# Performance work log

Measured on AMD Instinct MI355X. Metric: run time of the kernel, lower is better.

The kernel has to match this reference:

```python
import jax, jax.numpy as jnp
import numpy as np

N_NODES = 50000
N_EDGES = 800000
D = 128            # input_dim == output_dim (no zero-padding branch in GatedGraphConv)
N_ETYPES = 4
N_STEPS = 8
B = 50
MAX_NODES = 1400
HID = 256


def setup_inputs() -> dict:
    key = jax.random.key(0)
    ks = jax.random.split(key, 10)
    # ragged graph sizes: alternating 600 / 1400 nodes, sums exactly to N_NODES
    counts = np.tile(np.array([600, 1400], dtype=np.int32), B // 2)
    s_d = 1.0 / np.sqrt(D)
    s_h = 1.0 / np.sqrt(HID)
    return {
        "node_features": jax.random.normal(ks[0], (N_NODES, D), jnp.float32),
        "edge_src": jax.random.randint(ks[1], (N_EDGES,), 0, N_NODES, dtype=jnp.int32),
        "edge_dst": jax.random.randint(ks[2], (N_EDGES,), 0, N_NODES, dtype=jnp.int32),
        "edge_types": jax.random.randint(ks[3], (N_EDGES,), 0, N_ETYPES, dtype=jnp.int32),
        "node_counts": jnp.asarray(counts),
        # per-edge-type message linears (DGL: one nn.Linear(out,out) per etype)
        "W_msg": jax.random.normal(ks[4], (N_ETYPES, D, D), jnp.float32) * s_d,
        "b_msg": jnp.zeros((N_ETYPES, D), jnp.float32),
        # GRUCell params (torch gate order: r, z, n)
        "W_ih": jax.random.normal(ks[5], (3 * D, D), jnp.float32) * s_d,
        "W_hh": jax.random.normal(ks[6], (3 * D, D), jnp.float32) * s_d,
        "b_ih": jnp.zeros((3 * D,), jnp.float32),
        "b_hh": jnp.zeros((3 * D,), jnp.float32),
        # classifier: Linear(D,256) + ReLU + Linear(256,1) + sigmoid (dropout = identity at eval)
        "W1": jax.random.normal(ks[7], (D, HID), jnp.float32) * s_d,
        "b1": jnp.zeros((HID,), jnp.float32),
        "W2": jax.random.normal(ks[8], (HID, 1), jnp.float32) * s_h,
        "b2": jnp.zeros((1,), jnp.float32),
    }


def _forward(node_features, edge_src, edge_dst, edge_types, node_counts,
             W_msg, b_msg, W_ih, W_hh, b_ih, b_hh, W1, b1, W2, b2):
    h = node_features
    for _ in range(N_STEPS):
        h_src = h[edge_src]                                   # [E, D] gather
        m = jnp.zeros_like(h_src)
        for t in range(N_ETYPES):                             # small fixed loop over edge types
            m = m + jnp.where((edge_types == t)[:, None],
                              h_src @ W_msg[t] + b_msg[t], 0.0)
        a = jax.ops.segment_sum(m, edge_dst, num_segments=N_NODES)  # [N, D] scatter-sum
        # GRUCell update
        gi = a @ W_ih.T + b_ih
        gh = h @ W_hh.T + b_hh
        i_r, i_z, i_n = jnp.split(gi, 3, axis=-1)
        h_r, h_z, h_n = jnp.split(gh, 3, axis=-1)
        r = jax.nn.sigmoid(i_r + h_r)
        z = jax.nn.sigmoid(i_z + h_z)
        n = jnp.tanh(i_n + r * h_n)
        h = (1.0 - z) * n + z * h
    # de-batchify to padded [B, MAX_NODES, D] + masked mean pool
    offsets = jnp.concatenate([jnp.zeros((1,), node_counts.dtype),
                               jnp.cumsum(node_counts)[:-1]])
    idx = offsets[:, None] + jnp.arange(MAX_NODES, dtype=node_counts.dtype)
    mask = jnp.arange(MAX_NODES)[None, :] < node_counts[:, None]
    g = h[jnp.clip(idx, 0, N_NODES - 1)] * mask[..., None]    # [B, MAX_NODES, D]
    pooled = g.sum(axis=1) / node_counts[:, None].astype(h.dtype)
    x = jax.nn.relu(pooled @ W1 + b1)
    return jax.nn.sigmoid(x @ W2 + b2)                        # [B, 1]


def reference(node_features, edge_src, edge_dst, edge_types, node_counts,
              W_msg, b_msg, W_ih, W_hh, b_ih, b_hh, W1, b1, W2, b2):
    return _forward(node_features, edge_src, edge_dst, edge_types, node_counts,
                    W_msg, b_msg, W_ih, W_hh, b_ih, b_hh, W1, b1, W2, b2)
```

## Files before the change

kernel.cpp:

```cpp
#include <hip/hip_runtime.h>
#include <hip/hip_bf16.h>

#define N_NODES 50000
#define N_EDGES 800000
#define D 128
#define N_ETYPES 4
#define N_STEPS 8
#define B_GRAPHS 50
#define HID 256
#define POOL_SPLIT 16
#define N4 (N_NODES * N_ETYPES)
#define SCAN_B4 ((N4 + 255) / 256)

typedef __attribute__((ext_vector_type(8))) short short8;
typedef __attribute__((ext_vector_type(4))) float f32x4;
typedef __attribute__((ext_vector_type(4))) unsigned uint4v;
typedef __attribute__((ext_vector_type(4))) int int4v;

static __device__ __forceinline__ unsigned short f2bf(float f) {
    union { float f; unsigned u; } v; v.f = f;
    unsigned r = v.u + 0x7FFF + ((v.u >> 16) & 1);
    return (unsigned short)(r >> 16);
}
static __device__ __forceinline__ unsigned pk2(float a, float b) {
    return (unsigned)f2bf(a) | ((unsigned)f2bf(b) << 16);
}
static __device__ __forceinline__ float bf2f_u(unsigned s) {
    union { unsigned u; float f; } v; v.u = s << 16;
    return v.f;
}
static __device__ __forceinline__ float bflo(unsigned x) {
    union { unsigned u; float f; } v; v.u = x << 16;
    return v.f;
}
static __device__ __forceinline__ float bfhi(unsigned x) {
    union { unsigned u; float f; } v; v.u = x & 0xFFFF0000u;
    return v.f;
}
static __device__ __forceinline__ float fsigmoid(float x) {
    return 1.f / (1.f + __expf(-x));
}
static __device__ __forceinline__ float ftanh(float x) {
    return 2.f / (1.f + __expf(-2.f * x)) - 1.f;
}

__global__ void k_init_h(const float* __restrict__ nf, unsigned short* __restrict__ hbf) {
    int i = blockIdx.x * blockDim.x + threadIdx.x;
    if (i < N_NODES * D) hbf[i] = f2bf(nf[i]);
}

__global__ void k_hist(const int* __restrict__ dst, const int* __restrict__ et,
                       int* __restrict__ deg4) {
    int e = blockIdx.x * blockDim.x + threadIdx.x;
    if (e < N_EDGES) atomicAdd(&deg4[dst[e] * 4 + et[e]], 1);
}

__global__ __launch_bounds__(256) void k_scan1(const int* __restrict__ deg4,
                                               int* __restrict__ bsum) {
    __shared__ int tmp[256];
    int t = threadIdx.x;
    int i = blockIdx.x * 256 + t;
    tmp[t] = (i < N4) ? deg4[i] : 0;
    __syncthreads();
    for (int s = 128; s > 0; s >>= 1) {
        if (t < s) tmp[t] += tmp[t + s];
        __syncthreads();
    }
    if (t == 0) bsum[blockIdx.x] = tmp[0];
}

__global__ __launch_bounds__(1024) void k_scan2(const int* __restrict__ bsum,
                                                int* __restrict__ bpfx,
                                                int* __restrict__ rowptr4) {
    __shared__ int part[1024];
    int t = threadIdx.x;
    int v = (t < SCAN_B4) ? bsum[t] : 0;
    part[t] = v;
    __syncthreads();
    for (int off = 1; off < 1024; off <<= 1) {
        int u = (t >= off) ? part[t - off] : 0;
        __syncthreads();
        part[t] += u;
        __syncthreads();
    }
    if (t < SCAN_B4) bpfx[t] = part[t] - v;
    if (t == SCAN_B4 - 1) rowptr4[N4] = part[t];
}

__global__ __launch_bounds__(256) void k_scan3(const int* __restrict__ deg4,
                                               const int* __restrict__ bpfx,
                                               int* __restrict__ rowptr4,
                                               int* __restrict__ cursor4) {
    __shared__ int part[256];
    int t = threadIdx.x;
    int i = blockIdx.x * 256 + t;
    int v = (i < N4) ? deg4[i] : 0;
    part[t] = v;
    __syncthreads();
    for (int off = 1; off < 256; off <<= 1) {
        int u = (t >= off) ? part[t - off] : 0;
        __syncthreads();
        part[t] += u;
        __syncthreads();
    }
    if (i < N4) {
        int rp = bpfx[blockIdx.x] + part[t] - v;
        rowptr4[i] = rp;
        cursor4[i] = rp;
    }
}

__global__ void k_fill(const int* __restrict__ src, const int* __restrict__ dst,
                       const int* __restrict__ et, int* __restrict__ cursor4,
                       int* __restrict__ epack) {
    int e = blockIdx.x * blockDim.x + threadIdx.x;
    if (e < N_EDGES) {
        int slot = atomicAdd(&cursor4[dst[e] * 4 + et[e]], 1);
        epack[slot] = src[e] << 8;
    }
}

__global__ void k_pack(const float* __restrict__ Wmsg, const float* __restrict__ Wih,
                       const float* __restrict__ Whh, unsigned short* __restrict__ Pmsg,
                       unsigned short* __restrict__ Pih, unsigned short* __restrict__ Phh) {
    int bt = blockIdx.x;
    int l = threadIdx.x;
    if (bt < 128) {
        int nt = bt >> 4, kc = bt & 15;
        int n = nt * 16 + (l & 15);
        unsigned short* out = Pmsg + (((size_t)bt * 64 + l) * 8);
#pragma unroll
        for (int i = 0; i < 8; ++i) {
            int k = kc * 32 + ((l >> 4) << 3) + i;
            out[i] = f2bf(Wmsg[(size_t)(k >> 7) * (D * D) + (k & 127) * D + n]);
        }
        return;
    }
    const float* src;
    unsigned short* dstp;
    int id;
    if (bt < 224) { id = bt - 128; src = Wih; dstp = Pih; }
    else          { id = bt - 224; src = Whh; dstp = Phh; }
    int nt = id >> 2, c = id & 3;
    int n = nt * 16 + (l & 15);
    unsigned short* out = dstp + (((size_t)(nt * 4 + c) * 64 + l) * 8);
#pragma unroll
    for (int i = 0; i < 8; ++i) {
        int k = c * 32 + ((l >> 4) << 3) + i;
        out[i] = f2bf(src[n * D + k]);
    }
}

__global__ void k_pack_bias(const float* __restrict__ bih, const float* __restrict__ bhh,
                            float4* __restrict__ gb4) {
    int c = threadIdx.x;
    float4 g;
    g.x = bih[c] + bhh[c];
    g.y = bih[128 + c] + bhh[128 + c];
    g.z = bih[256 + c];
    g.w = bhh[256 + c];
    gb4[c] = g;
}

__global__ __launch_bounds__(256) void k_aggregate_s(const unsigned short* __restrict__ hold,
                                                     const int* __restrict__ rowptr4,
                                                     const int* __restrict__ epack,
                                                     unsigned short* __restrict__ S) {
    int w = threadIdx.x >> 6, l = threadIdx.x & 63;
    int v = blockIdx.x * 4 + w;
    if (v >= N_NODES) return;
    int4v b = *(const int4v*)(rowptr4 + v * 4);
    int b4 = rowptr4[v * 4 + 4];
    const char* hp = (const char*)hold + 4 * l;
    unsigned* Srow = (unsigned*)(S + (size_t)v * 512);
#pragma unroll
    for (int t = 0; t < 4; ++t) {
        int i  = (t == 0) ? b.x : (t == 1) ? b.y : (t == 2) ? b.z : b.w;
        int hi = (t == 0) ? b.y : (t == 1) ? b.z : (t == 2) ? b.w : b4;
        float a0 = 0.f, a1 = 0.f;
        for (; i + 4 <= hi; i += 4) {
            int s0 = epack[i], s1 = epack[i + 1], s2 = epack[i + 2], s3 = epack[i + 3];
            unsigned x0 = *(const unsigned*)(hp + s0);
            unsigned x1 = *(const unsigned*)(hp + s1);
            unsigned x2 = *(const unsigned*)(hp + s2);
            unsigned x3 = *(const unsigned*)(hp + s3);
            a0 += bflo(x0) + bflo(x1) + bflo(x2) + bflo(x3);
            a1 += bfhi(x0) + bfhi(x1) + bfhi(x2) + bfhi(x3);
        }
        if (i + 2 <= hi) {
            int s0 = epack[i], s1 = epack[i + 1];
            unsigned x0 = *(const unsigned*)(hp + s0);
            unsigned x1 = *(const unsigned*)(hp + s1);
            a0 += bflo(x0) + bflo(x1);
            a1 += bfhi(x0) + bfhi(x1);
            i += 2;
        }
        if (i < hi) {
            unsigned x0 = *(const unsigned*)(hp + epack[i]);
            a0 += bflo(x0);
            a1 += bfhi(x0);
        }
        Srow[t * 64 + l] = pk2(a0, a1);
    }
}

__global__ __launch_bounds__(256) void k_gemm_a(const unsigned short* __restrict__ S,
                                                const unsigned short* __restrict__ Pmsg,
                                                const int* __restrict__ rowptr4,
                                                const float* __restrict__ bmsg,
                                                unsigned short* __restrict__ abf) {
    int tid = threadIdx.x, w = tid >> 6, l = tid & 63;
    int base = (blockIdx.x >> 1) * 64 + w * 16;
    int nh = (blockIdx.x & 1) * 4;
    int lr = l & 15, kb = l >> 4;
    int arow = base + lr; if (arow >= N_NODES) arow = N_NODES - 1;
    const short8* Sr = (const short8*)(S + (size_t)arow * 512);
    short8 af[16];
#pragma unroll
    for (int kc = 0; kc < 16; ++kc) af[kc] = Sr[kc * 4 + kb];
    float dgf[4][4];
#pragma unroll
    for (int j = 0; j < 4; ++j) {
        int row = base + kb * 4 + j; if (row >= N_NODES) row = N_NODES - 1;
        int4v r4 = *(const int4v*)(rowptr4 + row * 4);
        int r5 = rowptr4[row * 4 + 4];
        dgf[j][0] = (float)(r4.y - r4.x);
        dgf[j][1] = (float)(r4.z - r4.y);
        dgf[j][2] = (float)(r4.w - r4.z);
        dgf[j][3] = (float)(r5 - r4.w);
    }
    const short8* Bp = (const short8*)Pmsg;
#pragma unroll
    for (int ntp = 0; ntp < 2; ++ntp) {
        int nt0 = nh + ntp * 2;
        f32x4 acc0 = {0.f, 0.f, 0.f, 0.f}, acc1 = {0.f, 0.f, 0.f, 0.f};
#pragma unroll
        for (int kc = 0; kc < 16; ++kc) {
            short8 b0 = Bp[(size_t)((nt0 + 0) * 16 + kc) * 64 + l];
            short8 b1 = Bp[(size_t)((nt0 + 1) * 16 + kc) * 64 + l];
            acc0 = __builtin_amdgcn_mfma_f32_16x16x32_bf16(af[kc], b0, acc0, 0, 0, 0);
            acc1 = __builtin_amdgcn_mfma_f32_16x16x32_bf16(af[kc], b1, acc1, 0, 0, 0);
        }
#pragma unroll
        for (int half = 0; half < 2; ++half) {
            f32x4 acc = half ? acc1 : acc0;
            int col = (nt0 + half) * 16 + lr;
            float b0 = bmsg[col], b1 = bmsg[128 + col], b2 = bmsg[256 + col], b3 = bmsg[384 + col];
#pragma unroll
            for (int j = 0; j < 4; ++j) {
                int row = base + kb * 4 + j;
                if (row < N_NODES) {
                    float bias = dgf[j][0] * b0 + dgf[j][1] * b1 + dgf[j][2] * b2 + dgf[j][3] * b3;
                    abf[(size_t)row * D + col] = f2bf(acc[j] + bias);
                }
            }
        }
    }
}

__global__ __launch_bounds__(256) void k_gru(const unsigned short* __restrict__ abf,
                                             const unsigned short* __restrict__ hold,
                                             unsigned short* __restrict__ hnew,
                                             const unsigned short* __restrict__ Pih,
                                             const unsigned short* __restrict__ Phh,
                                             const float4* __restrict__ gb4) {
    int tid = threadIdx.x, w = tid >> 6, l = tid & 63;
    int base = (blockIdx.x >> 1) * 64 + w * 16;
    int nt0 = (blockIdx.x & 1) * 4;
    int lr = l & 15, kb = l >> 4;
    int arow = base + lr; if (arow >= N_NODES) arow = N_NODES - 1;
    const short8* ar = (const short8*)(abf + (size_t)arow * D);
    const short8* hr = (const short8*)(hold + (size_t)arow * D);
    short8 afa[4], afh[4];
#pragma unroll
    for (int c = 0; c < 4; ++c) { afa[c] = ar[c * 4 + kb]; afh[c] = hr[c * 4 + kb]; }
    const short8* Bi = (const short8*)Pih;
    const short8* Bh = (const short8*)Phh;
#pragma unroll
    for (int ntl = 0; ntl < 4; ++ntl) {
        int nt = nt0 + ntl;
        f32x4 racc = {0.f, 0.f, 0.f, 0.f};
        f32x4 zacc = {0.f, 0.f, 0.f, 0.f};
        f32x4 giacc = {0.f, 0.f, 0.f, 0.f};
        f32x4 ghacc = {0.f, 0.f, 0.f, 0.f};
#pragma unroll
        for (int c = 0; c < 4; ++c) {
            short8 bir = Bi[((0 * 8 + nt) * 4 + c) * 64 + l];
            short8 bhr = Bh[((0 * 8 + nt) * 4 + c) * 64 + l];
            short8 biz = Bi[((1 * 8 + nt) * 4 + c) * 64 + l];
            short8 bhz = Bh[((1 * 8 + nt) * 4 + c) * 64 + l];
            short8 bin = Bi[((2 * 8 + nt) * 4 + c) * 64 + l];
            short8 bhn = Bh[((2 * 8 + nt) * 4 + c) * 64 + l];
            racc = __builtin_amdgcn_mfma_f32_16x16x32_bf16(afa[c], bir, racc, 0, 0, 0);
            racc = __builtin_amdgcn_mfma_f32_16x16x32_bf16(afh[c], bhr, racc, 0, 0, 0);
            zacc = __builtin_amdgcn_mfma_f32_16x16x32_bf16(afa[c], biz, zacc, 0, 0, 0);
            zacc = __builtin_amdgcn_mfma_f32_16x16x32_bf16(afh[c], bhz, zacc, 0, 0, 0);
            giacc = __builtin_amdgcn_mfma_f32_16x16x32_bf16(afa[c], bin, giacc, 0, 0, 0);
            ghacc = __builtin_amdgcn_mfma_f32_16x16x32_bf16(afh[c], bhn, ghacc, 0, 0, 0);
        }
        int col = nt * 16 + lr;
        float4 gb = gb4[col];
#pragma unroll
        for (int j = 0; j < 4; ++j) {
            int row = base + kb * 4 + j;
            if (row < N_NODES) {
                float rr = fsigmoid(racc[j] + gb.x);
                float zz = fsigmoid(zacc[j] + gb.y);
                float nn = ftanh(giacc[j] + gb.z + rr * (ghacc[j] + gb.w));
                size_t idx = (size_t)row * D + col;
                float hv = bf2f_u(hold[idx]);
                hnew[idx] = f2bf((1.f - zz) * nn + zz * hv);
            }
        }
    }
}

__global__ __launch_bounds__(256) void k_pool1(const unsigned short* __restrict__ hbf,
                                               const int* __restrict__ counts,
                                               float* __restrict__ partial) {
    __shared__ float tmp[256];
    int g = blockIdx.x / POOL_SPLIT;
    int j = blockIdx.x % POOL_SPLIT;
    int t = threadIdx.x;
    int offset = 0;
    for (int i = 0; i < g; ++i) offset += counts[i];
    int cnt = counts[g];
    int d = t & 127, half = t >> 7;
    float acc = 0.f;
    for (int r = 2 * j + half; r < cnt; r += 2 * POOL_SPLIT)
        acc += bf2f_u(hbf[(size_t)(offset + r) * D + d]);
    tmp[t] = acc;
    __syncthreads();
    if (t < D) partial[(size_t)(g * POOL_SPLIT + j) * D + t] = tmp[t] + tmp[t + 128];
}

__global__ __launch_bounds__(256) void k_pool2(const float* __restrict__ partial,
                                               const int* __restrict__ counts,
                                               const float* __restrict__ W1,
                                               const float* __restrict__ b1,
                                               const float* __restrict__ W2,
                                               const float* __restrict__ b2,
                                               float* __restrict__ out) {
    __shared__ float pooled[D];
    __shared__ float xh[HID];
    int g = blockIdx.x;
    int t = threadIdx.x;
    int cnt = counts[g];
    if (t < D) {
        float s = 0.f;
#pragma unroll
        for (int j = 0; j < POOL_SPLIT; ++j)
            s += partial[(size_t)(g * POOL_SPLIT + j) * D + t];
        pooled[t] = s / (float)cnt;
    }
    __syncthreads();
    float x = b1[t];
    for (int k = 0; k < D; ++k) x += pooled[k] * W1[k * HID + t];
    x = fmaxf(x, 0.f);
    xh[t] = x * W2[t];
    __syncthreads();
    for (int s = 128; s > 0; s >>= 1) {
        if (t < s) xh[t] += xh[t + s];
        __syncthreads();
    }
    if (t == 0) out[g] = 1.f / (1.f + __expf(-(xh[0] + b2[0])));
}

extern "C" void kernel_launch(void* const* d_in, const int* in_sizes, int n_in,
                              void* d_out, int out_size, void* d_ws, size_t ws_size,
                              hipStream_t stream) {
    const float* nf   = (const float*)d_in[0];
    const int* esrc   = (const int*)d_in[1];
    const int* edst   = (const int*)d_in[2];
    const int* etyp   = (const int*)d_in[3];
    const int* counts = (const int*)d_in[4];
    const float* Wmsg = (const float*)d_in[5];
    const float* bmsg = (const float*)d_in[6];
    const float* Wih  = (const float*)d_in[7];
    const float* Whh  = (const float*)d_in[8];
    const float* bih  = (const float*)d_in[9];
    const float* bhh  = (const float*)d_in[10];
    const float* W1   = (const float*)d_in[11];
    const float* b1   = (const float*)d_in[12];
    const float* W2   = (const float*)d_in[13];
    const float* b2   = (const float*)d_in[14];
    float* out = (float*)d_out;

    char* ws = (char*)d_ws;
    size_t off = 0;
    auto alloc = [&](size_t bytes) {
        void* p = ws + off;
        off = (off + bytes + 255) & ~(size_t)255;
        return p;
    };
    unsigned short* hbf0 = (unsigned short*)alloc((size_t)N_NODES * D * 2);
    unsigned short* hbf1 = (unsigned short*)alloc((size_t)N_NODES * D * 2);
    unsigned short* abf  = (unsigned short*)alloc((size_t)N_NODES * D * 2);
    unsigned short* S    = (unsigned short*)alloc((size_t)N_NODES * 512 * 2);
    unsigned short* Pmsg = (unsigned short*)alloc(128 * 64 * 8 * 2);
    unsigned short* Pih  = (unsigned short*)alloc(24 * 4 * 64 * 8 * 2);
    unsigned short* Phh  = (unsigned short*)alloc(24 * 4 * 64 * 8 * 2);
    float* gb4 = (float*)alloc(128 * 16);
    int* deg4    = (int*)alloc((size_t)N4 * 4);
    int* rowptr4 = (int*)alloc((size_t)(N4 + 1) * 4);
    int* cursor4 = (int*)alloc((size_t)N4 * 4);
    int* epack   = (int*)alloc((size_t)N_EDGES * 4);
    float* partial = (float*)alloc((size_t)B_GRAPHS * POOL_SPLIT * D * 4);
    int* bsum = (int*)alloc(SCAN_B4 * 4);
    int* bpfx = (int*)alloc(SCAN_B4 * 4);

    hipMemsetAsync(deg4, 0, (size_t)N4 * 4, stream);
    k_init_h<<<(N_NODES * D) / 256, 256, 0, stream>>>(nf, hbf0);
    k_hist<<<N_EDGES / 256, 256, 0, stream>>>(edst, etyp, deg4);
    k_scan1<<<SCAN_B4, 256, 0, stream>>>(deg4, bsum);
    k_scan2<<<1, 1024, 0, stream>>>(bsum, bpfx, rowptr4);
    k_scan3<<<SCAN_B4, 256, 0, stream>>>(deg4, bpfx, rowptr4, cursor4);
    k_fill<<<N_EDGES / 256, 256, 0, stream>>>(esrc, edst, etyp, cursor4, epack);
    k_pack<<<320, 64, 0, stream>>>(Wmsg, Wih, Whh, Pmsg, Pih, Phh);
    k_pack_bias<<<1, 128, 0, stream>>>(bih, bhh, (float4*)gb4);

    int ga_blocks  = 2 * ((N_NODES + 63) / 64);
    int gru_blocks = 2 * ((N_NODES + 63) / 64);
    int agg_blocks = (N_NODES + 3) / 4;
    for (int s = 0; s < N_STEPS; ++s) {
        const unsigned short* hold = (s & 1) ? hbf1 : hbf0;
        unsigned short* hnew       = (s & 1) ? hbf0 : hbf1;
        k_aggregate_s<<<agg_blocks, 256, 0, stream>>>(hold, rowptr4, epack, S);
        k_gemm_a<<<ga_blocks, 256, 0, stream>>>(S, Pmsg, rowptr4, bmsg, abf);
        k_gru<<<gru_blocks, 256, 0, stream>>>(abf, hold, hnew, Pih, Phh,
                                              (const float4*)gb4);
    }
    k_pool1<<<B_GRAPHS * POOL_SPLIT, 256, 0, stream>>>(hbf0, counts, partial);
    k_pool2<<<B_GRAPHS, 256, 0, stream>>>(partial, counts, W1, b1, W2, b2, out);
}
```

Before: 1.054 ms.

## Fuse message GEMM and GRU update into one kernel via LDS staging

Merges the per-step message-projection GEMM and the GRU kernel into a single kernel. Each wave computes its 16 rows of the aggregated message in full (all 8 column tiles), writes them as bf16 into an XOR-swizzled shared-memory tile, then reads them back as MFMA A-fragments for the GRU gates. This drops the global round trip of the intermediate activation buffer and one launch per step. In exchange, grid size is halved, since each block now covers all columns, and there is more work per block plus register pressure.

```diff
diff --git a/kernel.cpp b/kernel.cpp
--- a/kernel.cpp
+++ b/kernel.cpp
@@ -204,112 +204,112 @@
     }
 }
 
-__global__ __launch_bounds__(256) void k_gemm_a(const unsigned short* __restrict__ S,
-                                                const unsigned short* __restrict__ Pmsg,
-                                                const int* __restrict__ rowptr4,
-                                                const float* __restrict__ bmsg,
-                                                unsigned short* __restrict__ abf) {
+__global__ __launch_bounds__(256) void k_gau(const unsigned short* __restrict__ S,
+                                             const unsigned short* __restrict__ hold,
+                                             unsigned short* __restrict__ hnew,
+                                             const unsigned short* __restrict__ Pmsg,
+                                             const unsigned short* __restrict__ Pih,
+                                             const unsigned short* __restrict__ Phh,
+                                             const int* __restrict__ rowptr4,
+                                             const float* __restrict__ bmsg,
+                                             const float4* __restrict__ gb4) {
+    __shared__ unsigned short At[64 * 128];
     int tid = threadIdx.x, w = tid >> 6, l = tid & 63;
-    int base = (blockIdx.x >> 1) * 64 + w * 16;
-    int nh = (blockIdx.x & 1) * 4;
     int lr = l & 15, kb = l >> 4;
+    int base = blockIdx.x * 64 + w * 16;
     int arow = base + lr; if (arow >= N_NODES) arow = N_NODES - 1;
-    const short8* Sr = (const short8*)(S + (size_t)arow * 512);
-    short8 af[16];
-#pragma unroll
-    for (int kc = 0; kc < 16; ++kc) af[kc] = Sr[kc * 4 + kb];
-    float dgf[4][4];
-#pragma unroll
-    for (int j = 0; j < 4; ++j) {
-        int row = base + kb * 4 + j; if (row >= N_NODES) row = N_NODES - 1;
-        int4v r4 = *(const int4v*)(rowptr4 + row * 4);
-        int r5 = rowptr4[row * 4 + 4];
-        dgf[j][0] = (float)(r4.y - r4.x);
-        dgf[j][1] = (float)(r4.z - r4.y);
-        dgf[j][2] = (float)(r4.w - r4.z);
-        dgf[j][3] = (float)(r5 - r4.w);
-    }
-    const short8* Bp = (const short8*)Pmsg;
-#pragma unroll
-    for (int ntp = 0; ntp < 2; ++ntp) {
-        int nt0 = nh + ntp * 2;
-        f32x4 acc0 = {0.f, 0.f, 0.f, 0.f}, acc1 = {0.f, 0.f, 0.f, 0.f};
-#pragma unroll
-        for (int kc = 0; kc < 16; ++kc) {
-            short8 b0 = Bp[(size_t)((nt0 + 0) * 16 + kc) * 64 + l];
-            short8 b1 = Bp[(size_t)((nt0 + 1) * 16 + kc) * 64 + l];
-            acc0 = __builtin_amdgcn_mfma_f32_16x16x32_bf16(af[kc], b0, acc0, 0, 0, 0);
-            acc1 = __builtin_amdgcn_mfma_f32_16x16x32_bf16(af[kc], b1, acc1, 0, 0, 0);
-        }
-#pragma unroll
-        for (int half = 0; half < 2; ++half) {
-            f32x4 acc = half ? acc1 : acc0;
-            int col = (nt0 + half) * 16 + lr;
-            float b0 = bmsg[col], b1 = bmsg[128 + col], b2 = bmsg[256 + col], b3 = bmsg[384 + col];
+    char* myrows = (char*)At + (size_t)(w * 16) * 256;
+
+    {
+        const short8* Sr = (const short8*)(S + (size_t)arow * 512);
+        short8 af[16];
+#pragma unroll
+        for (int kc = 0; kc < 16; ++kc) af[kc] = Sr[kc * 4 + kb];
+        float dgf[4][4];
+#pragma unroll
+        for (int j = 0; j < 4; ++j) {
+            int row = base + kb * 4 + j; if (row >= N_NODES) row = N_NODES - 1;
+            int4v r4 = *(const int4v*)(rowptr4 + row * 4);
+            int r5 = rowptr4[row * 4 + 4];
+            dgf[j][0] = (float)(r4.y - r4.x);
+            dgf[j][1] = (float)(r4.z - r4.y);
+            dgf[j][2] = (float)(r4.w - r4.z);
+            dgf[j][3] = (float)(r5 - r4.w);
+        }
+        const short8* Bp = (const short8*)Pmsg;
+#pragma unroll
+        for (int ntp = 0; ntp < 4; ++ntp) {
+            f32x4 acc0 = {0.f, 0.f, 0.f, 0.f}, acc1 = {0.f, 0.f, 0.f, 0.f};
+#pragma unroll
+            for (int kc = 0; kc < 16; ++kc) {
+                short8 b0 = Bp[(size_t)((ntp * 2 + 0) * 16 + kc) * 64 + l];
+                short8 b1 = Bp[(size_t)((ntp * 2 + 1) * 16 + kc) * 64 + l];
+                acc0 = __builtin_amdgcn_mfma_f32_16x16x32_bf16(af[kc], b0, acc0, 0, 0, 0);
+                acc1 = __builtin_amdgcn_mfma_f32_16x16x32_bf16(af[kc], b1, acc1, 0, 0, 0);
+            }
+#pragma unroll
+            for (int half = 0; half < 2; ++half) {
+                f32x4 acc = half ? acc1 : acc0;
+                int nt = ntp * 2 + half;
+                int col = nt * 16 + lr;
+                float b0 = bmsg[col], b1 = bmsg[128 + col], b2 = bmsg[256 + col], b3 = bmsg[384 + col];
+#pragma unroll
+                for (int j = 0; j < 4; ++j) {
+                    int rl = kb * 4 + j;
+                    float av = acc[j] + dgf[j][0] * b0 + dgf[j][1] * b1 +
+                               dgf[j][2] * b2 + dgf[j][3] * b3;
+                    unsigned byte = (unsigned)(rl * 256 + col * 2) ^ ((unsigned)(rl & 7) << 4);
+                    *(unsigned short*)(myrows + byte) = f2bf(av);
+                }
+            }
+        }
+    }
+
+    {
+        const short8* hr = (const short8*)(hold + (size_t)arow * D);
+        short8 afh[4], afa[4];
+#pragma unroll
+        for (int c = 0; c < 4; ++c) {
+            afh[c] = hr[c * 4 + kb];
+            unsigned byte = (unsigned)(lr * 256 + c * 64 + kb * 16) ^ ((unsigned)(lr & 7) << 4);
+            afa[c] = *(const short8*)(myrows + byte);
+        }
+        const short8* Bi = (const short8*)Pih;
+        const short8* Bh = (const short8*)Phh;
+#pragma unroll
+        for (int nt = 0; nt < 8; ++nt) {
+            f32x4 racc = {0.f, 0.f, 0.f, 0.f};
+            f32x4 zacc = {0.f, 0.f, 0.f, 0.f};
+            f32x4 giacc = {0.f, 0.f, 0.f, 0.f};
+            f32x4 ghacc = {0.f, 0.f, 0.f, 0.f};
+#pragma unroll
+            for (int c = 0; c < 4; ++c) {
+                short8 bir = Bi[(size_t)((0 * 8 + nt) * 4 + c) * 64 + l];
+                short8 bhr = Bh[(size_t)((0 * 8 + nt) * 4 + c) * 64 + l];
+                short8 biz = Bi[(size_t)((1 * 8 + nt) * 4 + c) * 64 + l];
+                short8 bhz = Bh[(size_t)((1 * 8 + nt) * 4 + c) * 64 + l];
+                short8 bin = Bi[(size_t)((2 * 8 + nt) * 4 + c) * 64 + l];
+                short8 bhn = Bh[(size_t)((2 * 8 + nt) * 4 + c) * 64 + l];
+                racc = __builtin_amdgcn_mfma_f32_16x16x32_bf16(afa[c], bir, racc, 0, 0, 0);
+                racc = __builtin_amdgcn_mfma_f32_16x16x32_bf16(afh[c], bhr, racc, 0, 0, 0);
+                zacc = __builtin_amdgcn_mfma_f32_16x16x32_bf16(afa[c], biz, zacc, 0, 0, 0);
+                zacc = __builtin_amdgcn_mfma_f32_16x16x32_bf16(afh[c], bhz, zacc, 0, 0, 0);
+                giacc = __builtin_amdgcn_mfma_f32_16x16x32_bf16(afa[c], bin, giacc, 0, 0, 0);
+                ghacc = __builtin_amdgcn_mfma_f32_16x16x32_bf16(afh[c], bhn, ghacc, 0, 0, 0);
+            }
+            int col = nt * 16 + lr;
+            float4 gb = gb4[col];
 #pragma unroll
             for (int j = 0; j < 4; ++j) {
                 int row = base + kb * 4 + j;
                 if (row < N_NODES) {
-                    float bias = dgf[j][0] * b0 + dgf[j][1] * b1 + dgf[j][2] * b2 + dgf[j][3] * b3;
-                    abf[(size_t)row * D + col] = f2bf(acc[j] + bias);
+                    float rr = fsigmoid(racc[j] + gb.x);
+                    float zz = fsigmoid(zacc[j] + gb.y);
+                    float nn = ftanh(giacc[j] + gb.z + rr * (ghacc[j] + gb.w));
+                    size_t idx = (size_t)row * D + col;
+                    float hv = bf2f_u(hold[idx]);
+                    hnew[idx] = f2bf((1.f - zz) * nn + zz * hv);
                 }
-            }
-        }
-    }
-}
-
-__global__ __launch_bounds__(256) void k_gru(const unsigned short* __restrict__ abf,
-                                             const unsigned short* __restrict__ hold,
-                                             unsigned short* __restrict__ hnew,
-                                             const unsigned short* __restrict__ Pih,
-                                             const unsigned short* __restrict__ Phh,
-                                             const float4* __restrict__ gb4) {
-    int tid = threadIdx.x, w = tid >> 6, l = tid & 63;
-    int base = (blockIdx.x >> 1) * 64 + w * 16;
-    int nt0 = (blockIdx.x & 1) * 4;
-    int lr = l & 15, kb = l >> 4;
-    int arow = base + lr; if (arow >= N_NODES) arow = N_NODES - 1;
-    const short8* ar = (const short8*)(abf + (size_t)arow * D);
-    const short8* hr = (const short8*)(hold + (size_t)arow * D);
-    short8 afa[4], afh[4];
-#pragma unroll
-    for (int c = 0; c < 4; ++c) { afa[c] = ar[c * 4 + kb]; afh[c] = hr[c * 4 + kb]; }
-    const short8* Bi = (const short8*)Pih;
-    const short8* Bh = (const short8*)Phh;
-#pragma unroll
-    for (int ntl = 0; ntl < 4; ++ntl) {
-        int nt = nt0 + ntl;
-        f32x4 racc = {0.f, 0.f, 0.f, 0.f};
-        f32x4 zacc = {0.f, 0.f, 0.f, 0.f};
-        f32x4 giacc = {0.f, 0.f, 0.f, 0.f};
-        f32x4 ghacc = {0.f, 0.f, 0.f, 0.f};
-#pragma unroll
-        for (int c = 0; c < 4; ++c) {
-            short8 bir = Bi[((0 * 8 + nt) * 4 + c) * 64 + l];
-            short8 bhr = Bh[((0 * 8 + nt) * 4 + c) * 64 + l];
-            short8 biz = Bi[((1 * 8 + nt) * 4 + c) * 64 + l];
-            short8 bhz = Bh[((1 * 8 + nt) * 4 + c) * 64 + l];
-            short8 bin = Bi[((2 * 8 + nt) * 4 + c) * 64 + l];
-            short8 bhn = Bh[((2 * 8 + nt) * 4 + c) * 64 + l];
-            racc = __builtin_amdgcn_mfma_f32_16x16x32_bf16(afa[c], bir, racc, 0, 0, 0);
-            racc = __builtin_amdgcn_mfma_f32_16x16x32_bf16(afh[c], bhr, racc, 0, 0, 0);
-            zacc = __builtin_amdgcn_mfma_f32_16x16x32_bf16(afa[c], biz, zacc, 0, 0, 0);
-            zacc = __builtin_amdgcn_mfma_f32_16x16x32_bf16(afh[c], bhz, zacc, 0, 0, 0);
-            giacc = __builtin_amdgcn_mfma_f32_16x16x32_bf16(afa[c], bin, giacc, 0, 0, 0);
-            ghacc = __builtin_amdgcn_mfma_f32_16x16x32_bf16(afh[c], bhn, ghacc, 0, 0, 0);
-        }
-        int col = nt * 16 + lr;
-        float4 gb = gb4[col];
-#pragma unroll
-        for (int j = 0; j < 4; ++j) {
-            int row = base + kb * 4 + j;
-            if (row < N_NODES) {
-                float rr = fsigmoid(racc[j] + gb.x);
-                float zz = fsigmoid(zacc[j] + gb.y);
-                float nn = ftanh(giacc[j] + gb.z + rr * (ghacc[j] + gb.w));
-                size_t idx = (size_t)row * D + col;
-                float hv = bf2f_u(hold[idx]);
-                hnew[idx] = f2bf((1.f - zz) * nn + zz * hv);
             }
         }
     }
@@ -395,7 +395,6 @@
     };
     unsigned short* hbf0 = (unsigned short*)alloc((size_t)N_NODES * D * 2);
     unsigned short* hbf1 = (unsigned short*)alloc((size_t)N_NODES * D * 2);
-    unsigned short* abf  = (unsigned short*)alloc((size_t)N_NODES * D * 2);
     unsigned short* S    = (unsigned short*)alloc((size_t)N_NODES * 512 * 2);
     unsigned short* Pmsg = (unsigned short*)alloc(128 * 64 * 8 * 2);
     unsigned short* Pih  = (unsigned short*)alloc(24 * 4 * 64 * 8 * 2);
@@ -419,16 +418,14 @@
     k_pack<<<320, 64, 0, stream>>>(Wmsg, Wih, Whh, Pmsg, Pih, Phh);
     k_pack_bias<<<1, 128, 0, stream>>>(bih, bhh, (float4*)gb4);
 
-    int ga_blocks  = 2 * ((N_NODES + 63) / 64);
-    int gru_blocks = 2 * ((N_NODES + 63) / 64);
+    int gau_blocks = (N_NODES + 63) / 64;
     int agg_blocks = (N_NODES + 3) / 4;
     for (int s = 0; s < N_STEPS; ++s) {
         const unsigned short* hold = (s & 1) ? hbf1 : hbf0;
         unsigned short* hnew       = (s & 1) ? hbf0 : hbf1;
         k_aggregate_s<<<agg_blocks, 256, 0, stream>>>(hold, rowptr4, epack, S);
-        k_gemm_a<<<ga_blocks, 256, 0, stream>>>(S, Pmsg, rowptr4, bmsg, abf);
-        k_gru<<<gru_blocks, 256, 0, stream>>>(abf, hold, hnew, Pih, Phh,
-                                              (const float4*)gb4);
+        k_gau<<<gau_blocks, 256, 0, stream>>>(S, hold, hnew, Pmsg, Pih, Phh,
+                                              rowptr4, bmsg, (const float4*)gb4);
     }
     k_pool1<<<B_GRAPHS * POOL_SPLIT, 256, 0, stream>>>(hbf0, counts, partial);
     k_pool2<<<B_GRAPHS, 256, 0, stream>>>(partial, counts, W1, b1, W2, b2, out);
```

After: 1.149 ms. 1.09x slower.

## Remap GEMM and GRU blocks to 16 rows with waves splitting output columns

Applied to the files above, without the earlier changes.

k_gemm_a and k_gru now give each block 16 rows, with its four waves splitting the output column tiles, instead of 64 rows across waves and two column halves across blocks. The block count becomes N_NODES/16, which shrinks per-wave MFMA work and register use, and the four waves of a block share the same A-fragment rows in cache. Bounds checks are removed on the basis that N_NODES is divisible by 16 and by 4. Each wave still reloads its own A fragments, so redundant A reads per block grow, and the weight fragments are now loaded once per 16 rows.

```diff
diff --git a/kernel.cpp b/kernel.cpp
--- a/kernel.cpp
+++ b/kernel.cpp
@@ -168,7 +168,6 @@
                                                      unsigned short* __restrict__ S) {
     int w = threadIdx.x >> 6, l = threadIdx.x & 63;
     int v = blockIdx.x * 4 + w;
-    if (v >= N_NODES) return;
     int4v b = *(const int4v*)(rowptr4 + v * 4);
     int b4 = rowptr4[v * 4 + 4];
     const char* hp = (const char*)hold + 4 * l;
@@ -210,10 +209,9 @@
                                                 const float* __restrict__ bmsg,
                                                 unsigned short* __restrict__ abf) {
     int tid = threadIdx.x, w = tid >> 6, l = tid & 63;
-    int base = (blockIdx.x >> 1) * 64 + w * 16;
-    int nh = (blockIdx.x & 1) * 4;
     int lr = l & 15, kb = l >> 4;
-    int arow = base + lr; if (arow >= N_NODES) arow = N_NODES - 1;
+    int base = blockIdx.x * 16;
+    int arow = base + lr;
     const short8* Sr = (const short8*)(S + (size_t)arow * 512);
     short8 af[16];
 #pragma unroll
@@ -221,7 +219,7 @@
     float dgf[4][4];
 #pragma unroll
     for (int j = 0; j < 4; ++j) {
-        int row = base + kb * 4 + j; if (row >= N_NODES) row = N_NODES - 1;
+        int row = base + kb * 4 + j;
         int4v r4 = *(const int4v*)(rowptr4 + row * 4);
         int r5 = rowptr4[row * 4 + 4];
         dgf[j][0] = (float)(r4.y - r4.x);
@@ -230,30 +228,25 @@
         dgf[j][3] = (float)(r5 - r4.w);
     }
     const short8* Bp = (const short8*)Pmsg;
-#pragma unroll
-    for (int ntp = 0; ntp < 2; ++ntp) {
-        int nt0 = nh + ntp * 2;
-        f32x4 acc0 = {0.f, 0.f, 0.f, 0.f}, acc1 = {0.f, 0.f, 0.f, 0.f};
-#pragma unroll
-        for (int kc = 0; kc < 16; ++kc) {
-            short8 b0 = Bp[(size_t)((nt0 + 0) * 16 + kc) * 64 + l];
-            short8 b1 = Bp[(size_t)((nt0 + 1) * 16 + kc) * 64 + l];
-            acc0 = __builtin_amdgcn_mfma_f32_16x16x32_bf16(af[kc], b0, acc0, 0, 0, 0);
-            acc1 = __builtin_amdgcn_mfma_f32_16x16x32_bf16(af[kc], b1, acc1, 0, 0, 0);
-        }
-#pragma unroll
-        for (int half = 0; half < 2; ++half) {
-            f32x4 acc = half ? acc1 : acc0;
-            int col = (nt0 + half) * 16 + lr;
-            float b0 = bmsg[col], b1 = bmsg[128 + col], b2 = bmsg[256 + col], b3 = bmsg[384 + col];
-#pragma unroll
-            for (int j = 0; j < 4; ++j) {
-                int row = base + kb * 4 + j;
-                if (row < N_NODES) {
-                    float bias = dgf[j][0] * b0 + dgf[j][1] * b1 + dgf[j][2] * b2 + dgf[j][3] * b3;
-                    abf[(size_t)row * D + col] = f2bf(acc[j] + bias);
-                }
-            }
+    int nt0 = 2 * w;
+    f32x4 acc0 = {0.f, 0.f, 0.f, 0.f}, acc1 = {0.f, 0.f, 0.f, 0.f};
+#pragma unroll
+    for (int kc = 0; kc < 16; ++kc) {
+        short8 b0 = Bp[(size_t)((nt0 + 0) * 16 + kc) * 64 + l];
+        short8 b1 = Bp[(size_t)((nt0 + 1) * 16 + kc) * 64 + l];
+        acc0 = __builtin_amdgcn_mfma_f32_16x16x32_bf16(af[kc], b0, acc0, 0, 0, 0);
+        acc1 = __builtin_amdgcn_mfma_f32_16x16x32_bf16(af[kc], b1, acc1, 0, 0, 0);
+    }
+#pragma unroll
+    for (int half = 0; half < 2; ++half) {
+        f32x4 acc = half ? acc1 : acc0;
+        int col = (nt0 + half) * 16 + lr;
+        float b0 = bmsg[col], b1 = bmsg[128 + col], b2 = bmsg[256 + col], b3 = bmsg[384 + col];
+#pragma unroll
+        for (int j = 0; j < 4; ++j) {
+            int row = base + kb * 4 + j;
+            float bias = dgf[j][0] * b0 + dgf[j][1] * b1 + dgf[j][2] * b2 + dgf[j][3] * b3;
+            abf[(size_t)row * D + col] = f2bf(acc[j] + bias);
         }
     }
 }
@@ -265,10 +258,9 @@
                                              const unsigned short* __restrict__ Phh,
                                              const float4* __restrict__ gb4) {
     int tid = threadIdx.x, w = tid >> 6, l = tid & 63;
-    int base = (blockIdx.x >> 1) * 64 + w * 16;
-    int nt0 = (blockIdx.x & 1) * 4;
     int lr = l & 15, kb = l >> 4;
-    int arow = base + lr; if (arow >= N_NODES) arow = N_NODES - 1;
+    int base = blockIdx.x * 16;
+    int arow = base + lr;
     const short8* ar = (const short8*)(abf + (size_t)arow * D);
     const short8* hr = (const short8*)(hold + (size_t)arow * D);
     short8 afa[4], afh[4];
@@ -276,8 +268,9 @@
     for (int c = 0; c < 4; ++c) { afa[c] = ar[c * 4 + kb]; afh[c] = hr[c * 4 + kb]; }
     const short8* Bi = (const short8*)Pih;
     const short8* Bh = (const short8*)Phh;
-#pragma unroll
-    for (int ntl = 0; ntl < 4; ++ntl) {
+    int nt0 = 2 * w;
+#pragma unroll
+    for (int ntl = 0; ntl < 2; ++ntl) {
         int nt = nt0 + ntl;
         f32x4 racc = {0.f, 0.f, 0.f, 0.f};
         f32x4 zacc = {0.f, 0.f, 0.f, 0.f};
@@ -285,12 +278,12 @@
         f32x4 ghacc = {0.f, 0.f, 0.f, 0.f};
 #pragma unroll
         for (int c = 0; c < 4; ++c) {
-            short8 bir = Bi[((0 * 8 + nt) * 4 + c) * 64 + l];
-            short8 bhr = Bh[((0 * 8 + nt) * 4 + c) * 64 + l];
-            short8 biz = Bi[((1 * 8 + nt) * 4 + c) * 64 + l];
-            short8 bhz = Bh[((1 * 8 + nt) * 4 + c) * 64 + l];
-            short8 bin = Bi[((2 * 8 + nt) * 4 + c) * 64 + l];
-            short8 bhn = Bh[((2 * 8 + nt) * 4 + c) * 64 + l];
+            short8 bir = Bi[(size_t)((0 * 8 + nt) * 4 + c) * 64 + l];
+            short8 bhr = Bh[(size_t)((0 * 8 + nt) * 4 + c) * 64 + l];
+            short8 biz = Bi[(size_t)((1 * 8 + nt) * 4 + c) * 64 + l];
+            short8 bhz = Bh[(size_t)((1 * 8 + nt) * 4 + c) * 64 + l];
+            short8 bin = Bi[(size_t)((2 * 8 + nt) * 4 + c) * 64 + l];
+            short8 bhn = Bh[(size_t)((2 * 8 + nt) * 4 + c) * 64 + l];
             racc = __builtin_amdgcn_mfma_f32_16x16x32_bf16(afa[c], bir, racc, 0, 0, 0);
             racc = __builtin_amdgcn_mfma_f32_16x16x32_bf16(afh[c], bhr, racc, 0, 0, 0);
             zacc = __builtin_amdgcn_mfma_f32_16x16x32_bf16(afa[c], biz, zacc, 0, 0, 0);
@@ -303,14 +296,12 @@
 #pragma unroll
         for (int j = 0; j < 4; ++j) {
             int row = base + kb * 4 + j;
-            if (row < N_NODES) {
-                float rr = fsigmoid(racc[j] + gb.x);
-                float zz = fsigmoid(zacc[j] + gb.y);
-                float nn = ftanh(giacc[j] + gb.z + rr * (ghacc[j] + gb.w));
-                size_t idx = (size_t)row * D + col;
-                float hv = bf2f_u(hold[idx]);
-                hnew[idx] = f2bf((1.f - zz) * nn + zz * hv);
-            }
+            float rr = fsigmoid(racc[j] + gb.x);
+            float zz = fsigmoid(zacc[j] + gb.y);
+            float nn = ftanh(giacc[j] + gb.z + rr * (ghacc[j] + gb.w));
+            size_t idx = (size_t)row * D + col;
+            float hv = bf2f_u(hold[idx]);
+            hnew[idx] = f2bf((1.f - zz) * nn + zz * hv);
         }
     }
 }
@@ -419,16 +410,15 @@
     k_pack<<<320, 64, 0, stream>>>(Wmsg, Wih, Whh, Pmsg, Pih, Phh);
     k_pack_bias<<<1, 128, 0, stream>>>(bih, bhh, (float4*)gb4);
 
-    int ga_blocks  = 2 * ((N_NODES + 63) / 64);
-    int gru_blocks = 2 * ((N_NODES + 63) / 64);
-    int agg_blocks = (N_NODES + 3) / 4;
+    int gemm_blocks = N_NODES / 16;
+    int agg_blocks  = (N_NODES + 3) / 4;
     for (int s = 0; s < N_STEPS; ++s) {
         const unsigned short* hold = (s & 1) ? hbf1 : hbf0;
         unsigned short* hnew       = (s & 1) ? hbf0 : hbf1;
         k_aggregate_s<<<agg_blocks, 256, 0, stream>>>(hold, rowptr4, epack, S);
-        k_gemm_a<<<ga_blocks, 256, 0, stream>>>(S, Pmsg, rowptr4, bmsg, abf);
-        k_gru<<<gru_blocks, 256, 0, stream>>>(abf, hold, hnew, Pih, Phh,
-                                              (const float4*)gb4);
+        k_gemm_a<<<gemm_blocks, 256, 0, stream>>>(S, Pmsg, rowptr4, bmsg, abf);
+        k_gru<<<gemm_blocks, 256, 0, stream>>>(abf, hold, hnew, Pih, Phh,
+                                               (const float4*)gb4);
     }
     k_pool1<<<B_GRAPHS * POOL_SPLIT, 256, 0, stream>>>(hbf0, counts, partial);
     k_pool2<<<B_GRAPHS, 256, 0, stream>>>(partial, counts, W1, b1, W2, b2, out);
```

Result: slower. 1.083 ms (+2.7%).
